# Kernel tuning notes

Hardware: AMD Instinct MI355X
Metric: run time of the kernel (lower is better)

Reference implementation:

```python
import jax, jax.numpy as jnp
import numpy as np

B, C, S, H, NC = 256, 2000, 50, 64, 3


def setup_inputs() -> dict:
    key = jax.random.key(0)
    ks = jax.random.split(key, 7)
    s = 1.0 / np.sqrt(H)  # PyTorch LSTM init scale
    return {
        "x": jax.random.normal(ks[0], (B, C, S), dtype=jnp.float32),
        "W_ih": jax.random.uniform(ks[1], (4 * H, 1), jnp.float32, -s, s),
        "W_hh": jax.random.uniform(ks[2], (4 * H, H), jnp.float32, -s, s),
        "b_ih": jax.random.uniform(ks[3], (4 * H,), jnp.float32, -s, s),
        "b_hh": jax.random.uniform(ks[4], (4 * H,), jnp.float32, -s, s),
        "W_fc": jax.random.uniform(ks[5], (NC, H), jnp.float32, -s, s),
        "b_fc": jax.random.uniform(ks[6], (NC,), jnp.float32, -s, s),
    }


def _lstm_last_h(x_flat, W_ih, W_hh, b_ih, b_hh):
    # x_flat: [N, S, 1] with N = B*C. PyTorch gate order: i, f, g, o.
    N = x_flat.shape[0]
    b = b_ih + b_hh  # [4H]
    # input_dim == 1, so precompute the input contribution for all steps:
    # [N, S, 1] @ [1, 4H] -> [N, S, 4H], then scan over time axis.
    x_proj = x_flat @ W_ih.T + b  # [N, S, 4H]
    xs = jnp.moveaxis(x_proj, 1, 0)  # [S, N, 4H]

    def step(carry, x_t):
        h, c = carry
        gates = x_t + h @ W_hh.T  # [N, 4H]
        i, f, g, o = jnp.split(gates, 4, axis=-1)
        i = jax.nn.sigmoid(i)
        f = jax.nn.sigmoid(f)
        g = jnp.tanh(g)
        o = jax.nn.sigmoid(o)
        c = f * c + i * g
        h = o * jnp.tanh(c)
        return (h, c), None

    h0 = jnp.zeros((N, x_proj.shape[-1] // 4), x_flat.dtype)
    (h_last, _), _ = jax.lax.scan(step, (h0, h0), xs)
    return h_last  # [N, H]


def reference(x, W_ih, W_hh, b_ih, b_hh, W_fc, b_fc):
    Bsz, Nc, Sl = x.shape
    x_flat = x.reshape(Bsz * Nc, Sl, 1)
    h_last = _lstm_last_h(x_flat, W_ih, W_hh, b_ih, b_hh)  # [B*C, H]
    logits = h_last @ W_fc.T + b_fc  # [B*C, NC]
    return logits.reshape(Bsz, Nc, -1)
```

## Files before the change

kernel.cpp:

```cpp
#include <hip/hip_runtime.h>

typedef _Float16 h8 __attribute__((ext_vector_type(8)));
typedef _Float16 h4 __attribute__((ext_vector_type(4)));
typedef float f4 __attribute__((ext_vector_type(4)));

#define SEQ_LEN 50
#define HID 64
#define HS 72

#if __has_builtin(__builtin_amdgcn_exp2f)
#define EXP2(x) __builtin_amdgcn_exp2f(x)
#else
extern "C" __device__ float __ocml_native_exp2_f32(float);
#define EXP2(x) __ocml_native_exp2_f32(x)
#endif
#define RCP(x) __builtin_amdgcn_rcpf(x)

#define LOG2E  1.442695041f
#define LOG2E2 2.885390082f

__global__ __launch_bounds__(128, 3)
void lstm_fused(const float* __restrict__ x,
                const float* __restrict__ W_ih,
                const float* __restrict__ W_hh,
                const float* __restrict__ b_ih,
                const float* __restrict__ b_hh,
                const float* __restrict__ W_fc,
                const float* __restrict__ b_fc,
                float* __restrict__ out)
{
    __shared__ _Float16 sH[2][16 * HS];
    __shared__ float    sXT[SEQ_LEN * 16];

    const int tid  = threadIdx.x;
    const int wave = tid >> 6;
    const int lane = tid & 63;
    const int col  = lane & 15;
    const int quad = lane >> 4;
    const int seqBase = blockIdx.x << 4;

    for (int i = tid; i < SEQ_LEN * 16; i += 128) {
        const int s = i & 15;
        const int t = i >> 4;
        sXT[t * 16 + s] = x[(size_t)(seqBase + s) * SEQ_LEN + t];
    }
    for (int i = tid; i < 2 * 16 * HS; i += 128)
        ((_Float16*)sH)[i] = (_Float16)0.0f;

    h8 Aw[8][2];
    h8 Ax[8];
    #pragma unroll
    for (int gi = 0; gi < 4; ++gi) {
        const float scale = (gi == 2) ? LOG2E2 : LOG2E;
        #pragma unroll
        for (int d = 0; d < 2; ++d) {
            const int tt = gi * 2 + d;
            const int n  = (gi * 4 + 2 * wave + d) * 16 + col;
            h8 axf = {};
            if (quad == 0) {
                axf[0] = (_Float16)(W_ih[n] * scale);
                axf[1] = (_Float16)((b_ih[n] + b_hh[n]) * scale);
            }
            Ax[tt] = axf;
            #pragma unroll
            for (int kf = 0; kf < 2; ++kf) {
                const float* wp = W_hh + n * HID + kf * 32 + quad * 8;
                f4 lo = *(const f4*)wp;
                f4 hi = *(const f4*)(wp + 4);
                h8 b;
                b[0] = (_Float16)(lo[0] * scale); b[1] = (_Float16)(lo[1] * scale);
                b[2] = (_Float16)(lo[2] * scale); b[3] = (_Float16)(lo[3] * scale);
                b[4] = (_Float16)(hi[0] * scale); b[5] = (_Float16)(hi[1] * scale);
                b[6] = (_Float16)(hi[2] * scale); b[7] = (_Float16)(hi[3] * scale);
                Aw[tt][kf] = b;
            }
        }
    }

    const f4 z4 = {0.0f, 0.0f, 0.0f, 0.0f};

    float c[2][4];
    #pragma unroll
    for (int d = 0; d < 2; ++d)
        #pragma unroll
        for (int r = 0; r < 4; ++r) c[d][r] = 0.0f;

    __syncthreads();

    #pragma unroll 2
    for (int t = 0; t < SEQ_LEN; ++t) {
        const _Float16* hb = sH[t & 1];
        _Float16*       hw = sH[(t + 1) & 1];

        const float xt = sXT[t * 16 + col];
        h8 bx = {};
        bx[0] = (_Float16)xt;
        bx[1] = (_Float16)1.0f;

        const h8 Bh0 = *(const h8*)(hb + col * HS + quad * 8);
        const h8 Bh1 = *(const h8*)(hb + col * HS + 32 + quad * 8);

        #pragma unroll
        for (int d = 0; d < 2; ++d) {
            f4 acc[4];
            #pragma unroll
            for (int gi = 0; gi < 4; ++gi) {
                const int tt = gi * 2 + d;
                f4 a = __builtin_amdgcn_mfma_f32_16x16x32_f16(Ax[tt], bx, z4, 0, 0, 0);
                a = __builtin_amdgcn_mfma_f32_16x16x32_f16(Aw[tt][0], Bh0, a, 0, 0, 0);
                a = __builtin_amdgcn_mfma_f32_16x16x32_f16(Aw[tt][1], Bh1, a, 0, 0, 0);
                acc[gi] = a;
            }
            h4 hv;
            #pragma unroll
            for (int r = 0; r < 4; ++r) {
                float Ei = EXP2(-acc[0][r]);
                float Ef = EXP2(-acc[1][r]);
                float Eg = EXP2( acc[2][r]);
                float Eo = EXP2(-acc[3][r]);
                float pi_ = 1.0f + Ei;
                float pf_ = 1.0f + Ef;
                float pg_ = 1.0f + Eg;
                float po_ = 1.0f + Eo;
                float t1  = pi_ * pg_;
                float v   = fmaf(Eg, LOG2E2, -LOG2E2) * pf_;
                float num = fmaf(c[d][r], t1, v);
                float rc  = RCP(pf_ * t1);
                float cn  = fminf(num * rc, 126.0f);
                c[d][r] = cn;
                float Ec  = EXP2(cn);
                float rh  = RCP(po_ * (1.0f + Ec));
                hv[r] = (_Float16)((Ec - 1.0f) * rh);
            }
            *(h4*)(hw + col * HS + 32 * wave + 16 * d + quad * 4) = hv;
        }
        __syncthreads();
    }

    if (lane < 24) {
        const int sl = wave * 8 + lane / 3;
        const int nc = lane % 3;
        const _Float16* hp = sH[0] + sl * HS;
        float a = b_fc[nc];
        #pragma unroll
        for (int u = 0; u < HID; ++u)
            a = fmaf((float)hp[u], W_fc[nc * HID + u], a);
        out[(size_t)(seqBase + sl) * 3 + nc] = a;
    }
}

extern "C" void kernel_launch(void* const* d_in, const int* in_sizes, int n_in,
                              void* d_out, int out_size, void* d_ws, size_t ws_size,
                              hipStream_t stream) {
    const float* x    = (const float*)d_in[0];
    const float* W_ih = (const float*)d_in[1];
    const float* W_hh = (const float*)d_in[2];
    const float* b_ih = (const float*)d_in[3];
    const float* b_hh = (const float*)d_in[4];
    const float* W_fc = (const float*)d_in[5];
    const float* b_fc = (const float*)d_in[6];
    float* out = (float*)d_out;

    const int nSeq   = in_sizes[0] / SEQ_LEN;
    const int blocks = nSeq / 16;

    hipLaunchKernelGGL(lstm_fused, dim3(blocks), dim3(128), 0, stream,
                       x, W_ih, W_hh, b_ih, b_hh, W_fc, b_fc, out);
}
```

Measured before the change: 1.790 ms.

## Process 32 sequences per block, reusing register-resident weights across two tiles

```diff
diff --git a/kernel.cpp b/kernel.cpp
--- a/kernel.cpp
+++ b/kernel.cpp
@@ -7,6 +7,7 @@
 #define SEQ_LEN 50
 #define HID 64
 #define HS 72
+#define NSEQ 32
 
 #if __has_builtin(__builtin_amdgcn_exp2f)
 #define EXP2(x) __builtin_amdgcn_exp2f(x)
@@ -19,7 +20,7 @@
 #define LOG2E  1.442695041f
 #define LOG2E2 2.885390082f
 
-__global__ __launch_bounds__(128, 3)
+__global__ __launch_bounds__(128, 2)
 void lstm_fused(const float* __restrict__ x,
                 const float* __restrict__ W_ih,
                 const float* __restrict__ W_hh,
@@ -29,22 +30,22 @@
                 const float* __restrict__ b_fc,
                 float* __restrict__ out)
 {
-    __shared__ _Float16 sH[2][16 * HS];
-    __shared__ float    sXT[SEQ_LEN * 16];
+    __shared__ _Float16 sH[2][NSEQ * HS];
+    __shared__ float    sXT[SEQ_LEN * NSEQ];
 
     const int tid  = threadIdx.x;
     const int wave = tid >> 6;
     const int lane = tid & 63;
     const int col  = lane & 15;
     const int quad = lane >> 4;
-    const int seqBase = blockIdx.x << 4;
+    const int seqBase = blockIdx.x * NSEQ;
 
-    for (int i = tid; i < SEQ_LEN * 16; i += 128) {
-        const int s = i & 15;
-        const int t = i >> 4;
-        sXT[t * 16 + s] = x[(size_t)(seqBase + s) * SEQ_LEN + t];
+    for (int i = tid; i < SEQ_LEN * NSEQ; i += 128) {
+        const int s = i & (NSEQ - 1);
+        const int t = i >> 5;
+        sXT[t * NSEQ + s] = x[(size_t)(seqBase + s) * SEQ_LEN + t];
     }
-    for (int i = tid; i < 2 * 16 * HS; i += 128)
+    for (int i = tid; i < 2 * NSEQ * HS; i += 128)
         ((_Float16*)sH)[i] = (_Float16)0.0f;
 
     h8 Aw[8][2];
@@ -79,67 +80,83 @@
 
     const f4 z4 = {0.0f, 0.0f, 0.0f, 0.0f};
 
-    float c[2][4];
+    float c[2][2][4];
     #pragma unroll
     for (int d = 0; d < 2; ++d)
         #pragma unroll
-        for (int r = 0; r < 4; ++r) c[d][r] = 0.0f;
+        for (int n = 0; n < 2; ++n)
+            #pragma unroll
+            for (int r = 0; r < 4; ++r) c[d][n][r] = 0.0f;
 
     __syncthreads();
 
-    #pragma unroll 2
     for (int t = 0; t < SEQ_LEN; ++t) {
         const _Float16* hb = sH[t & 1];
         _Float16*       hw = sH[(t + 1) & 1];
 
-        const float xt = sXT[t * 16 + col];
-        h8 bx = {};
-        bx[0] = (_Float16)xt;
-        bx[1] = (_Float16)1.0f;
+        h8 bx[2];
+        #pragma unroll
+        for (int n = 0; n < 2; ++n) {
+            h8 b = {};
+            b[0] = (_Float16)sXT[t * NSEQ + n * 16 + col];
+            b[1] = (_Float16)1.0f;
+            bx[n] = b;
+        }
 
-        const h8 Bh0 = *(const h8*)(hb + col * HS + quad * 8);
-        const h8 Bh1 = *(const h8*)(hb + col * HS + 32 + quad * 8);
+        h8 Bh[2][2];
+        #pragma unroll
+        for (int n = 0; n < 2; ++n) {
+            const _Float16* p = hb + (n * 16 + col) * HS + quad * 8;
+            Bh[n][0] = *(const h8*)p;
+            Bh[n][1] = *(const h8*)(p + 32);
+        }
 
         #pragma unroll
         for (int d = 0; d < 2; ++d) {
-            f4 acc[4];
+            f4 acc[4][2];
             #pragma unroll
             for (int gi = 0; gi < 4; ++gi) {
                 const int tt = gi * 2 + d;
-                f4 a = __builtin_amdgcn_mfma_f32_16x16x32_f16(Ax[tt], bx, z4, 0, 0, 0);
-                a = __builtin_amdgcn_mfma_f32_16x16x32_f16(Aw[tt][0], Bh0, a, 0, 0, 0);
-                a = __builtin_amdgcn_mfma_f32_16x16x32_f16(Aw[tt][1], Bh1, a, 0, 0, 0);
-                acc[gi] = a;
+                #pragma unroll
+                for (int n = 0; n < 2; ++n) {
+                    f4 a = __builtin_amdgcn_mfma_f32_16x16x32_f16(Ax[tt], bx[n], z4, 0, 0, 0);
+                    a = __builtin_amdgcn_mfma_f32_16x16x32_f16(Aw[tt][0], Bh[n][0], a, 0, 0, 0);
+                    a = __builtin_amdgcn_mfma_f32_16x16x32_f16(Aw[tt][1], Bh[n][1], a, 0, 0, 0);
+                    acc[gi][n] = a;
+                }
             }
-            h4 hv;
             #pragma unroll
-            for (int r = 0; r < 4; ++r) {
-                float Ei = EXP2(-acc[0][r]);
-                float Ef = EXP2(-acc[1][r]);
-                float Eg = EXP2( acc[2][r]);
-                float Eo = EXP2(-acc[3][r]);
-                float pi_ = 1.0f + Ei;
-                float pf_ = 1.0f + Ef;
-                float pg_ = 1.0f + Eg;
-                float po_ = 1.0f + Eo;
-                float t1  = pi_ * pg_;
-                float v   = fmaf(Eg, LOG2E2, -LOG2E2) * pf_;
-                float num = fmaf(c[d][r], t1, v);
-                float rc  = RCP(pf_ * t1);
-                float cn  = fminf(num * rc, 126.0f);
-                c[d][r] = cn;
-                float Ec  = EXP2(cn);
-                float rh  = RCP(po_ * (1.0f + Ec));
-                hv[r] = (_Float16)((Ec - 1.0f) * rh);
+            for (int n = 0; n < 2; ++n) {
+                h4 hv;
+                #pragma unroll
+                for (int r = 0; r < 4; ++r) {
+                    float Ei = EXP2(-acc[0][n][r]);
+                    float Ef = EXP2(-acc[1][n][r]);
+                    float Eg = EXP2( acc[2][n][r]);
+                    float Eo = EXP2(-acc[3][n][r]);
+                    float pi_ = 1.0f + Ei;
+                    float pf_ = 1.0f + Ef;
+                    float pg_ = 1.0f + Eg;
+                    float po_ = 1.0f + Eo;
+                    float t1  = pi_ * pg_;
+                    float v   = fmaf(Eg, LOG2E2, -LOG2E2) * pf_;
+                    float num = fmaf(c[d][n][r], t1, v);
+                    float rc  = RCP(pf_ * t1);
+                    float cn  = fminf(num * rc, 126.0f);
+                    c[d][n][r] = cn;
+                    float Ec  = EXP2(cn);
+                    float rh  = RCP(po_ * (1.0f + Ec));
+                    hv[r] = (_Float16)((Ec - 1.0f) * rh);
+                }
+                *(h4*)(hw + (n * 16 + col) * HS + 32 * wave + 16 * d + quad * 4) = hv;
             }
-            *(h4*)(hw + col * HS + 32 * wave + 16 * d + quad * 4) = hv;
         }
         __syncthreads();
     }
 
-    if (lane < 24) {
-        const int sl = wave * 8 + lane / 3;
-        const int nc = lane % 3;
+    if (tid < NSEQ * 3) {
+        const int sl = tid / 3;
+        const int nc = tid % 3;
         const _Float16* hp = sH[0] + sl * HS;
         float a = b_fc[nc];
         #pragma unroll
@@ -162,7 +179,7 @@
     float* out = (float*)d_out;
 
     const int nSeq   = in_sizes[0] / SEQ_LEN;
-    const int blocks = nSeq / 16;
+    const int blocks = nSeq / NSEQ;
 
     hipLaunchKernelGGL(lstm_fused, dim3(blocks), dim3(128), 0, stream,
                        x, W_ih, W_hh, b_ih, b_hh, W_fc, b_fc, out);
```

After: 1.849 ms. +3.3%, slower.

## Give each wave independent sequences with full hidden state and drop block barriers

Applied to the files above, without the earlier changes.

```diff
diff --git a/kernel.cpp b/kernel.cpp
--- a/kernel.cpp
+++ b/kernel.cpp
@@ -19,7 +19,7 @@
 #define LOG2E  1.442695041f
 #define LOG2E2 2.885390082f
 
-__global__ __launch_bounds__(128, 3)
+__global__ __launch_bounds__(256, 2)
 void lstm_fused(const float* __restrict__ x,
                 const float* __restrict__ W_ih,
                 const float* __restrict__ W_hh,
@@ -29,39 +29,41 @@
                 const float* __restrict__ b_fc,
                 float* __restrict__ out)
 {
-    __shared__ _Float16 sH[2][16 * HS];
-    __shared__ float    sXT[SEQ_LEN * 16];
+    __shared__ _Float16 sH[4][16 * HS];
+    __shared__ float    sXT[4][SEQ_LEN * 16];
 
     const int tid  = threadIdx.x;
     const int wave = tid >> 6;
     const int lane = tid & 63;
     const int col  = lane & 15;
     const int quad = lane >> 4;
-    const int seqBase = blockIdx.x << 4;
+    const int seqBase = blockIdx.x * 64 + wave * 16;
 
-    for (int i = tid; i < SEQ_LEN * 16; i += 128) {
+    _Float16* hbuf = sH[wave];
+    float*    xbuf = sXT[wave];
+
+    for (int i = lane; i < SEQ_LEN * 16; i += 64) {
         const int s = i & 15;
         const int t = i >> 4;
-        sXT[t * 16 + s] = x[(size_t)(seqBase + s) * SEQ_LEN + t];
+        xbuf[t * 16 + s] = x[(size_t)(seqBase + s) * SEQ_LEN + t];
     }
-    for (int i = tid; i < 2 * 16 * HS; i += 128)
-        ((_Float16*)sH)[i] = (_Float16)0.0f;
+    for (int i = lane; i < 16 * HS; i += 64)
+        hbuf[i] = (_Float16)0.0f;
 
-    h8 Aw[8][2];
-    h8 Ax[8];
+    h8 Aw[4][4][2];
+    h8 Ax[4][4];
     #pragma unroll
     for (int gi = 0; gi < 4; ++gi) {
         const float scale = (gi == 2) ? LOG2E2 : LOG2E;
         #pragma unroll
-        for (int d = 0; d < 2; ++d) {
-            const int tt = gi * 2 + d;
-            const int n  = (gi * 4 + 2 * wave + d) * 16 + col;
+        for (int dt = 0; dt < 4; ++dt) {
+            const int n = gi * 64 + dt * 16 + col;
             h8 axf = {};
             if (quad == 0) {
                 axf[0] = (_Float16)(W_ih[n] * scale);
                 axf[1] = (_Float16)((b_ih[n] + b_hh[n]) * scale);
             }
-            Ax[tt] = axf;
+            Ax[gi][dt] = axf;
             #pragma unroll
             for (int kf = 0; kf < 2; ++kf) {
                 const float* wp = W_hh + n * HID + kf * 32 + quad * 8;
@@ -72,43 +74,36 @@
                 b[2] = (_Float16)(lo[2] * scale); b[3] = (_Float16)(lo[3] * scale);
                 b[4] = (_Float16)(hi[0] * scale); b[5] = (_Float16)(hi[1] * scale);
                 b[6] = (_Float16)(hi[2] * scale); b[7] = (_Float16)(hi[3] * scale);
-                Aw[tt][kf] = b;
+                Aw[gi][dt][kf] = b;
             }
         }
     }
 
     const f4 z4 = {0.0f, 0.0f, 0.0f, 0.0f};
 
-    float c[2][4];
+    float c[4][4];
     #pragma unroll
-    for (int d = 0; d < 2; ++d)
+    for (int dt = 0; dt < 4; ++dt)
         #pragma unroll
-        for (int r = 0; r < 4; ++r) c[d][r] = 0.0f;
+        for (int r = 0; r < 4; ++r) c[dt][r] = 0.0f;
 
-    __syncthreads();
-
-    #pragma unroll 2
     for (int t = 0; t < SEQ_LEN; ++t) {
-        const _Float16* hb = sH[t & 1];
-        _Float16*       hw = sH[(t + 1) & 1];
-
-        const float xt = sXT[t * 16 + col];
         h8 bx = {};
-        bx[0] = (_Float16)xt;
+        bx[0] = (_Float16)xbuf[t * 16 + col];
         bx[1] = (_Float16)1.0f;
 
-        const h8 Bh0 = *(const h8*)(hb + col * HS + quad * 8);
-        const h8 Bh1 = *(const h8*)(hb + col * HS + 32 + quad * 8);
+        const _Float16* hp = hbuf + col * HS + quad * 8;
+        const h8 Bh0 = *(const h8*)hp;
+        const h8 Bh1 = *(const h8*)(hp + 32);
 
         #pragma unroll
-        for (int d = 0; d < 2; ++d) {
+        for (int dt = 0; dt < 4; ++dt) {
             f4 acc[4];
             #pragma unroll
             for (int gi = 0; gi < 4; ++gi) {
-                const int tt = gi * 2 + d;
-                f4 a = __builtin_amdgcn_mfma_f32_16x16x32_f16(Ax[tt], bx, z4, 0, 0, 0);
-                a = __builtin_amdgcn_mfma_f32_16x16x32_f16(Aw[tt][0], Bh0, a, 0, 0, 0);
-                a = __builtin_amdgcn_mfma_f32_16x16x32_f16(Aw[tt][1], Bh1, a, 0, 0, 0);
+                f4 a = __builtin_amdgcn_mfma_f32_16x16x32_f16(Ax[gi][dt], bx, z4, 0, 0, 0);
+                a = __builtin_amdgcn_mfma_f32_16x16x32_f16(Aw[gi][dt][0], Bh0, a, 0, 0, 0);
+                a = __builtin_amdgcn_mfma_f32_16x16x32_f16(Aw[gi][dt][1], Bh1, a, 0, 0, 0);
                 acc[gi] = a;
             }
             h4 hv;
@@ -124,23 +119,22 @@
                 float po_ = 1.0f + Eo;
                 float t1  = pi_ * pg_;
                 float v   = fmaf(Eg, LOG2E2, -LOG2E2) * pf_;
-                float num = fmaf(c[d][r], t1, v);
+                float num = fmaf(c[dt][r], t1, v);
                 float rc  = RCP(pf_ * t1);
                 float cn  = fminf(num * rc, 126.0f);
-                c[d][r] = cn;
+                c[dt][r] = cn;
                 float Ec  = EXP2(cn);
                 float rh  = RCP(po_ * (1.0f + Ec));
                 hv[r] = (_Float16)((Ec - 1.0f) * rh);
             }
-            *(h4*)(hw + col * HS + 32 * wave + 16 * d + quad * 4) = hv;
+            *(h4*)(hbuf + col * HS + dt * 16 + quad * 4) = hv;
         }
-        __syncthreads();
     }
 
-    if (lane < 24) {
-        const int sl = wave * 8 + lane / 3;
+    if (lane < 48) {
+        const int sl = lane / 3;
         const int nc = lane % 3;
-        const _Float16* hp = sH[0] + sl * HS;
+        const _Float16* hp = hbuf + sl * HS;
         float a = b_fc[nc];
         #pragma unroll
         for (int u = 0; u < HID; ++u)
@@ -162,8 +156,8 @@
     float* out = (float*)d_out;
 
     const int nSeq   = in_sizes[0] / SEQ_LEN;
-    const int blocks = nSeq / 16;
+    const int blocks = nSeq / 64;
 
-    hipLaunchKernelGGL(lstm_fused, dim3(blocks), dim3(128), 0, stream,
+    hipLaunchKernelGGL(lstm_fused, dim3(blocks), dim3(256), 0, stream,
                        x, W_ih, W_hh, b_ih, b_hh, W_fc, b_fc, out);
 }
```

Result: slower. 1.895 ms (+5.9%).
